# Optimization experiments

Hardware: AMD Instinct MI355X
Metric: run time of the kernel (lower is better)

The kernel has to match this reference:

```python
import jax, jax.numpy as jnp
import numpy as np
from jax import lax


def conv2d(x, w, b=None, pad=0):
    out = lax.conv_general_dilated(x, w, (1, 1), [(pad, pad), (pad, pad)],
                                   dimension_numbers=('NCHW', 'OIHW', 'NCHW'))
    return out if b is None else out + b[None, :, None, None]


def bn_inf(x, gamma, beta, mean, var, eps=1e-5):
    inv = gamma / jnp.sqrt(var + eps)
    return x * inv[None, :, None, None] + (beta - mean * inv)[None, :, None, None]


def silu(x):
    return x * jax.nn.sigmoid(x)


def deform_conv2d(x, offset, weight, groups):
    # torchvision DeformConv2d v1 semantics: kernel 3x3, stride 1, pad 1, dilation 1,
    # one offset group; offset channels interleaved (dy, dx) per kernel tap, row-major taps.
    B, C, H, W = x.shape
    K = 9
    off = offset.reshape(B, K, 2, H, W)
    dy, dx = off[:, :, 0], off[:, :, 1]                      # (B,K,H,W)
    ki = (jnp.arange(K) // 3 - 1).astype(x.dtype)            # kernel row offset (pad=1)
    kj = (jnp.arange(K) % 3 - 1).astype(x.dtype)
    py = jnp.arange(H, dtype=x.dtype)[None, None, :, None] + ki[None, :, None, None] + dy
    px = jnp.arange(W, dtype=x.dtype)[None, None, None, :] + kj[None, :, None, None] + dx
    y0 = jnp.floor(py)
    x0 = jnp.floor(px)
    wy1 = py - y0                                            # bilinear weights
    wx1 = px - x0
    y0i = y0.astype(jnp.int32)
    x0i = x0.astype(jnp.int32)
    xf = x.reshape(B, C, H * W)

    def gather(yi, xi):
        valid = ((yi >= 0) & (yi < H) & (xi >= 0) & (xi < W)).astype(x.dtype)
        idx = (jnp.clip(yi, 0, H - 1) * W + jnp.clip(xi, 0, W - 1)).reshape(B, K * H * W)
        v = jax.vmap(lambda f, i: jnp.take(f, i, axis=-1))(xf, idx).reshape(B, C, K, H, W)
        return v * valid[:, None]

    cols = (gather(y0i, x0i) * ((1 - wy1) * (1 - wx1))[:, None]
            + gather(y0i, x0i + 1) * ((1 - wy1) * wx1)[:, None]
            + gather(y0i + 1, x0i) * (wy1 * (1 - wx1))[:, None]
            + gather(y0i + 1, x0i + 1) * (wy1 * wx1)[:, None])   # (B,C,K,H,W)

    G = groups
    Cg = C // G
    Co = weight.shape[0]
    cols = cols.reshape(B, G, Cg, K, H, W)
    wg = weight.reshape(G, Co // G, Cg, K)
    return jnp.einsum('bgckhw,gock->bgohw', cols, wg).reshape(B, Co, H, W)


def d_clem_forward(x, x_prev, w_off, b_off, w_def, w_cross, w_g1, b_g1,
                   g1_gamma, g1_beta, g1_mean, g1_var, w_g2, b_g2,
                   w_out, b_out, o_gamma, o_beta, o_mean, o_var):
    offset = conv2d(x, w_off, b_off, pad=1)
    x_dir = deform_conv2d(x, offset, w_def, groups=4)
    x_dense = conv2d(jnp.concatenate([x_dir, x_prev], axis=1), w_cross, None, pad=0)
    a = silu(bn_inf(conv2d(x_dense, w_g1, b_g1, pad=1), g1_gamma, g1_beta, g1_mean, g1_var))
    attn = jax.nn.sigmoid(conv2d(a, w_g2, b_g2, pad=0))
    out = silu(bn_inf(conv2d(x_dense * attn, w_out, b_out, pad=0), o_gamma, o_beta, o_mean, o_var))
    return x + out  # use_residual: in_channels == out_channels


def setup_inputs() -> dict:
    key = jax.random.key(0)
    ks = jax.random.split(key, 16)
    B, C, H, W, G = 4, 256, 64, 64, 4

    def wt(k, shape, fan_in):
        return jax.random.normal(k, shape, jnp.float32) / np.float32(np.sqrt(fan_in))

    return {
        'x': jax.random.normal(ks[0], (B, C, H, W), jnp.float32),
        'x_prev': jax.random.normal(ks[1], (B, C, H, W), jnp.float32),
        'w_off': wt(ks[2], (18, C, 3, 3), C * 9),
        'b_off': 0.01 * jax.random.normal(ks[3], (18,), jnp.float32),
        'w_def': wt(ks[4], (C, C // G, 3, 3), (C // G) * 9),
        'w_cross': wt(ks[5], (C, 2 * C, 1, 1), 2 * C),
        'w_g1': wt(ks[6], (C // 4, C, 3, 3), C * 9),
        'b_g1': 0.01 * jax.random.normal(ks[7], (C // 4,), jnp.float32),
        'g1_gamma': 1.0 + 0.1 * jax.random.normal(ks[8], (C // 4,), jnp.float32),
        'g1_beta': 0.1 * jax.random.normal(ks[9], (C // 4,), jnp.float32),
        'g1_mean': 0.1 * jax.random.normal(ks[10], (C // 4,), jnp.float32),
        'g1_var': 0.5 + jax.random.uniform(ks[11], (C // 4,), jnp.float32),
        'w_g2': wt(ks[12], (C, C // 4, 1, 1), C // 4),
        'b_g2': jnp.zeros((C,), jnp.float32),
        'w_out': wt(ks[13], (C, C, 1, 1), C),
        'b_out': jnp.zeros((C,), jnp.float32),
        'o_gamma': 1.0 + 0.1 * jax.random.normal(ks[14], (C,), jnp.float32),
        'o_beta': jnp.zeros((C,), jnp.float32),
        'o_mean': 0.1 * jax.random.normal(ks[15], (C,), jnp.float32),
        'o_var': 0.5 + jax.random.uniform(jax.random.fold_in(key, 99), (C,), jnp.float32),
    }


def reference(x, x_prev, w_off, b_off, w_def, w_cross, w_g1, b_g1,
              g1_gamma, g1_beta, g1_mean, g1_var, w_g2, b_g2,
              w_out, b_out, o_gamma, o_beta, o_mean, o_var):
    return d_clem_forward(x, x_prev, w_off, b_off, w_def, w_cross, w_g1, b_g1,
                          g1_gamma, g1_beta, g1_mean, g1_var, w_g2, b_g2,
                          w_out, b_out, o_gamma, o_beta, o_mean, o_var)
```

## Files before the change

kernel.cpp:

```cpp
#include <hip/hip_runtime.h>
#include <hip/hip_bf16.h>

using bf16 = __hip_bfloat16;
typedef __attribute__((ext_vector_type(8))) short short8;
typedef __attribute__((ext_vector_type(4))) float f32x4;

__device__ __forceinline__ float b2f(bf16 v){ return __bfloat162float(v); }
__device__ __forceinline__ float sigf(float v){ return 1.f/(1.f + __expf(-v)); }
__device__ __forceinline__ float ldv(const float* p, int i){ return p[i]; }
__device__ __forceinline__ float ldv(const bf16* p, int i){ return b2f(p[i]); }
__device__ __forceinline__ void stv(float* p, int i, float v){ p[i] = v; }
__device__ __forceinline__ void stv(bf16* p, int i, float v){ p[i] = __float2bfloat16(v); }
__device__ __forceinline__ float bfe(short8 v, int j){
  unsigned short s = (unsigned short)v[j];
  return b2f(*(bf16*)&s);
}

__device__ __forceinline__ void ld2v(const float* p, float& a, float& b){
  float2 v = *(const float2*)p; a = v.x; b = v.y;
}
__device__ __forceinline__ void ld2v(const bf16* p, float& a, float& b){
  unsigned int u = *(const unsigned int*)p;
  unsigned short s0 = (unsigned short)(u & 0xFFFF), s1 = (unsigned short)(u >> 16);
  a = b2f(*(bf16*)&s0); b = b2f(*(bf16*)&s1);
}
__device__ __forceinline__ void ld8(const bf16* s, unsigned int* pk){
  short8 v = *(const short8*)s;
  #pragma unroll
  for (int e = 0; e < 4; e++)
    pk[e] = (unsigned int)(unsigned short)v[2*e]
          | ((unsigned int)(unsigned short)v[2*e+1] << 16);
}
__device__ __forceinline__ void ld8(const float* s, unsigned int* pk){
  f32x4 a = *(const f32x4*)s, c = *(const f32x4*)(s + 4);
  float vals[8] = {a[0],a[1],a[2],a[3],c[0],c[1],c[2],c[3]};
  #pragma unroll
  for (int e = 0; e < 4; e++){
    bf16 h0 = __float2bfloat16(vals[2*e]), h1 = __float2bfloat16(vals[2*e+1]);
    pk[e] = (unsigned int)*(unsigned short*)&h0
          | ((unsigned int)*(unsigned short*)&h1 << 16);
  }
}

__global__ __launch_bounds__(256) void k_detect(const unsigned short* xs, int* flag){
  __shared__ int cnt;
  if (threadIdx.x == 0) cnt = 0;
  __syncthreads();
  int local = 0;
  for (int i = threadIdx.x; i < 16384; i += 256){
    if (((xs[i] >> 7) & 0xFF) == 0xFF) local++;
  }
  if (local) atomicAdd(&cnt, local);
  __syncthreads();
  if (threadIdx.x == 0) *flag = (cnt > 0) ? 1 : 0;
}

struct ParamSrc { const void* p[18]; };

__global__ __launch_bounds__(256) void k_convert(ParamSrc ps, const int* flagp,
    float* cpar, bf16* wdefb, bf16* woffb, bf16* wg1b, bf16* wcrossb, bf16* woutb,
    float* cwT){
  static constexpr int n[24]   = {41472,18,147456,131072,147456,64,64,64,64,64,
                                  16384,256,65536,256,256,256,256,256,
                                  147456,73728,147456,131072,65536,16384};
  static constexpr int off[18] = {0,41472,41504,188960,320032,467488,467552,467616,
                                  467680,467744,467808,484192,484448,549984,550240,
                                  550496,550752,551008};
  const int s = blockIdx.y;
  const bool f32 = (*flagp != 0);
  if (s == 23){
    for (int i = blockIdx.x * 256 + threadIdx.x; i < 16384; i += gridDim.x * 256){
      const int c = i >> 8, co = i & 255;
      if (f32) cwT[i] = ((const float*)ps.p[10])[co * 64 + c];
      else     cwT[i] = b2f(((const bf16*)ps.p[10])[co * 64 + c]);
    }
    return;
  }
  if (s >= 18){
    static constexpr int srcs[5] = {2, 0, 4, 3, 12};
    const int src_slot = srcs[s - 18];
    bf16* dst = (s == 18) ? wdefb : (s == 19) ? woffb : (s == 20) ? wg1b
              : (s == 21) ? wcrossb : woutb;
    const int nsrc = (s == 19) ? 41472 : n[s];
    const bool remap = (s == 19 || s == 20);
    for (int i = blockIdx.x * 256 + threadIdx.x; i < n[s]; i += gridDim.x * 256){
      int srcIdx = i;
      if (remap){
        const int co = i / 2304, rem = i % 2304;
        const int chunk = rem / 288, r2 = rem % 288;
        const int tap = r2 >> 5, cl = r2 & 31;
        srcIdx = co * 2304 + (chunk * 32 + cl) * 9 + tap;
      }
      if (f32){
        const float* src = (const float*)ps.p[src_slot];
        dst[i] = (srcIdx < nsrc) ? __float2bfloat16(src[srcIdx]) : __float2bfloat16(0.f);
      } else {
        const bf16* src = (const bf16*)ps.p[src_slot];
        dst[i] = (srcIdx < nsrc) ? src[srcIdx] : __float2bfloat16(0.f);
      }
    }
    return;
  }
  float* dst = cpar + off[s];
  if (f32){
    const float* src = (const float*)ps.p[s];
    for (int i = blockIdx.x * 256 + threadIdx.x; i < n[s]; i += gridDim.x * 256)
      dst[i] = src[i];
  } else {
    const bf16* src = (const bf16*)ps.p[s];
    for (int i = blockIdx.x * 256 + threadIdx.x; i < n[s]; i += gridDim.x * 256)
      dst[i] = b2f(src[i]);
  }
}

template<typename T>
__device__ __forceinline__ void xt_body(const T* __restrict__ x, bf16* __restrict__ xt){
  __shared__ float lds[64][65];
  const int bx = blockIdx.x;
  const int b = bx >> 8, y = (bx >> 2) & 63, g = bx & 3;
  const int t = threadIdx.x;
  const int px = t & 63, cq = t >> 6;
  #pragma unroll
  for (int it = 0; it < 16; it++){
    const int ch = cq * 16 + it;
    lds[ch][px] = ldv(x, ((b * 256 + g * 64 + ch) * 64 + y) * 64 + px);
  }
  __syncthreads();
  const int ch = t & 63, pb = t >> 6;
  bf16* ob = xt + ((b * 4 + g) * 4096 + y * 64) * 64 + ch;
  #pragma unroll
  for (int i = 0; i < 16; i++){
    const int p = pb * 16 + i;
    ob[p * 64] = __float2bfloat16(lds[ch][p]);
  }
}

__global__ __launch_bounds__(256) void k_xt(const void* x, const int* flagp, bf16* xt){
  if (*flagp) xt_body((const float*)x, xt);
  else        xt_body((const bf16*)x, xt);
}

template<typename T, int COT>
__device__ __forceinline__ void conv3_raw(const T* __restrict__ xin,
    const bf16* __restrict__ wb, float* __restrict__ outp, int co_lim,
    unsigned short* xt16, int cc_begin){
  const int bx = blockIdx.x;
  const int b = bx >> 6, y = bx & 63;
  const int t = threadIdx.x;
  const int l = t & 63, w = t >> 6;
  const int lm = l & 15, lq = l >> 4;
  const int px = w * 16 + lm;
  f32x4 acc[COT];
  #pragma unroll
  for (int m = 0; m < COT; m++) acc[m] = (f32x4){0.f,0.f,0.f,0.f};

  #pragma unroll
  for (int ch_i = 0; ch_i < 2; ch_i++){
    const int cc = cc_begin + ch_i * 32;
    __syncthreads();
    if (t < 96){
      const int c = t / 3, r = t - c * 3;
      xt16[c * 210 + r * 70 + 3]  = 0;
      xt16[c * 210 + r * 70 + 68] = 0;
    }
    #pragma unroll
    for (int it = 0; it < 3; it++){
      const int u = t + it * 256;
      const int pb = u & 7;
      const int cr = u >> 3;
      const int c = cr / 3, r = cr - c * 3;
      const int yy = y + r - 1;
      const int px0 = pb * 8;
      unsigned int pk[4];
      if ((unsigned)yy < 64u){
        ld8(xin + (b * 256 + cc + c) * 4096 + yy * 64 + px0, pk);
      } else {
        pk[0] = pk[1] = pk[2] = pk[3] = 0;
      }
      unsigned int* dp = (unsigned int*)(xt16 + c * 210 + r * 70 + 4 + px0);
      dp[0] = pk[0]; dp[1] = pk[1]; dp[2] = pk[2]; dp[3] = pk[3];
    }
    __syncthreads();
    const int chunkG = cc >> 5;
    const unsigned short* bt = xt16 + 3 + px;
    #pragma unroll
    for (int tap = 0; tap < 9; tap++){
      const int ti = tap / 3, tj = tap - ti * 3;
      short8 bfr;
      #pragma unroll
      for (int j = 0; j < 8; j++)
        bfr[j] = (short)bt[(lq * 8 + j) * 210 + ti * 70 + tj];
      #pragma unroll
      for (int m = 0; m < COT; m++){
        const bf16* ap = wb + (m * 16 + lm) * 2304 + chunkG * 288 + tap * 32 + lq * 8;
        short8 afr = *(const short8*)ap;
        acc[m] = __builtin_amdgcn_mfma_f32_16x16x32_bf16(afr, bfr, acc[m], 0, 0, 0);
      }
    }
  }
  const int p = y * 64 + px;
  #pragma unroll
  for (int m = 0; m < COT; m++){
    #pragma unroll
    for (int r = 0; r < 4; r++){
      const int co = m * 16 + lq * 4 + r;
      if (co >= co_lim) continue;
      outp[(b * co_lim + co) * 4096 + p] = acc[m][r];
    }
  }
}

__global__ __launch_bounds__(256) void k_coff_m(const void* x, const int* flagp,
    const bf16* woffb, float* offp){
  __shared__ __align__(16) unsigned short xtile[32 * 210];
  float* op = offp + blockIdx.y * 294912;
  const int cc0 = blockIdx.y * 64;
  if (*flagp) conv3_raw<float, 2>((const float*)x, woffb, op, 18, xtile, cc0);
  else        conv3_raw<bf16, 2>((const bf16*)x, woffb, op, 18, xtile, cc0);
}

__global__ __launch_bounds__(256) void k_g1_m(const bf16* xdense,
    const bf16* wg1b, float* abp){
  __shared__ __align__(16) unsigned short xtile[32 * 210];
  float* op = abp + blockIdx.y * 1048576;
  conv3_raw<bf16, 4>(xdense, wg1b, op, 64, xtile, blockIdx.y * 64);
}

__global__ __launch_bounds__(256) void k_omerge(const float* __restrict__ offp,
    const float* __restrict__ cb, float* __restrict__ offc){
  const int i4 = (blockIdx.x * 256 + threadIdx.x) * 4;
  constexpr int PS = 294912;
  f32x4 a = *(const f32x4*)(offp + i4);
  f32x4 b = *(const f32x4*)(offp + PS + i4);
  f32x4 c = *(const f32x4*)(offp + 2 * PS + i4);
  f32x4 d = *(const f32x4*)(offp + 3 * PS + i4);
  const int co = (i4 >> 12) % 18;
  const float bias = cb[co];
  f32x4 r;
  #pragma unroll
  for (int j = 0; j < 4; j++) r[j] = ((a[j] + b[j]) + c[j]) + d[j] + bias;
  *(f32x4*)(offc + i4) = r;
}

#define CROWM 600

__global__ __launch_bounds__(256) void k_deform(const bf16* __restrict__ xt,
    const float* __restrict__ offc, const bf16* __restrict__ wdefb,
    bf16* __restrict__ xdir){
  __shared__ __align__(16) unsigned short cols[32 * CROWM];
  const int g = blockIdx.y;
  const int q0 = blockIdx.x * 32;
  const int b = q0 >> 12, p0 = q0 & 4095;
  const int t = threadIdx.x;
  {
    const int pos = t & 31, u8 = t >> 5;
    const int c0 = u8 * 8;
    const int p = p0 + pos;
    const int y = p >> 6, xx = p & 63;
    const float* ob = offc + b * 18 * 4096 + p;
    const bf16* xg = xt + (b * 4 + g) * 4096 * 64;
    #pragma unroll
    for (int k = 0; k < 9; k++){
      float dy = ob[(2 * k) * 4096];
      float dx = ob[(2 * k + 1) * 4096];
      float py = (float)(y + k / 3 - 1) + dy;
      float px = (float)(xx + k % 3 - 1) + dx;
      float y0f = floorf(py), x0f = floorf(px);
      int y0 = (int)y0f, x0 = (int)x0f;
      float wy1 = py - y0f, wx1 = px - x0f;
      float wy0 = 1.f - wy1, wx0 = 1.f - wx1;
      bool vy0 = (unsigned)y0 < 64u, vy1 = (unsigned)(y0 + 1) < 64u;
      bool vx0 = (unsigned)x0 < 64u, vx1 = (unsigned)(x0 + 1) < 64u;
      float w00 = (vy0 && vx0) ? wy0 * wx0 : 0.f;
      float w01 = (vy0 && vx1) ? wy0 * wx1 : 0.f;
      float w10 = (vy1 && vx0) ? wy1 * wx0 : 0.f;
      float w11 = (vy1 && vx1) ? wy1 * wx1 : 0.f;
      int yc0 = min(max(y0, 0), 63), yc1 = min(max(y0 + 1, 0), 63);
      int xc0 = min(max(x0, 0), 63), xc1 = min(max(x0 + 1, 0), 63);
      int i00 = yc0 * 64 + xc0, i01 = yc0 * 64 + xc1;
      int i10 = yc1 * 64 + xc0, i11 = yc1 * 64 + xc1;
      short8 s00 = *(const short8*)(xg + i00 * 64 + c0);
      short8 s01 = *(const short8*)(xg + i01 * 64 + c0);
      short8 s10 = *(const short8*)(xg + i10 * 64 + c0);
      short8 s11 = *(const short8*)(xg + i11 * 64 + c0);
      #pragma unroll
      for (int j = 0; j < 8; j++){
        float val = w00 * bfe(s00, j) + w01 * bfe(s01, j)
                  + w10 * bfe(s10, j) + w11 * bfe(s11, j);
        bf16 hv = __float2bfloat16(val);
        cols[pos * CROWM + (c0 + j) * 9 + k] = *(unsigned short*)&hv;
      }
    }
  }
  __syncthreads();
  {
    const int w = t >> 6;
    const int l = t & 63;
    const int lrow = l & 15;
    const int lhi = l >> 4;
    f32x4 acc0 = {0.f, 0.f, 0.f, 0.f};
    f32x4 acc1 = {0.f, 0.f, 0.f, 0.f};
    const bf16* wr = wdefb + (g * 64 + w * 16 + lrow) * 576;
    const unsigned short* b0p = cols + lrow * CROWM;
    const unsigned short* b1p = cols + (16 + lrow) * CROWM;
    #pragma unroll 2
    for (int kk = 0; kk < 576; kk += 32){
      int ko = kk + lhi * 8;
      short8 a  = *(const short8*)(wr + ko);
      short8 b0 = *(const short8*)(b0p + ko);
      short8 b1 = *(const short8*)(b1p + ko);
      acc0 = __builtin_amdgcn_mfma_f32_16x16x32_bf16(a, b0, acc0, 0, 0, 0);
      acc1 = __builtin_amdgcn_mfma_f32_16x16x32_bf16(a, b1, acc1, 0, 0, 0);
    }
    const int co_base = g * 64 + w * 16 + lhi * 4;
    #pragma unroll
    for (int r = 0; r < 4; r++){
      bf16* xo = xdir + (b * 256 + co_base + r) * 4096 + p0 + lrow;
      xo[0]  = __float2bfloat16(acc0[r]);
      xo[16] = __float2bfloat16(acc1[r]);
    }
  }
}

template<typename T>
__device__ __forceinline__ void cross_load(const bf16* __restrict__ xdir,
    const T* __restrict__ xprev, int b, int y, int pos2, int cq, int cc,
    unsigned int* pk){
  #pragma unroll
  for (int c8 = 0; c8 < 8; c8++){
    const int ci = cc + cq * 8 + c8;
    if (ci < 256){
      pk[c8] = *(const unsigned int*)(xdir + (b * 256 + ci) * 4096 + y * 64 + 2 * pos2);
    } else {
      float v0, v1;
      ld2v(xprev + (b * 256 + (ci - 256)) * 4096 + y * 64 + 2 * pos2, v0, v1);
      bf16 h0 = __float2bfloat16(v0), h1 = __float2bfloat16(v1);
      pk[c8] = (unsigned int)*(unsigned short*)&h0
             | ((unsigned int)*(unsigned short*)&h1 << 16);
    }
  }
}

template<typename T>
__device__ __forceinline__ void cross_mfma_body(const bf16* __restrict__ xdir,
    const T* __restrict__ xprev, const bf16* __restrict__ wb,
    bf16* __restrict__ xdense, unsigned short* cols){
  const int bx = blockIdx.x;
  const int b = bx >> 6, y = bx & 63;
  const int co0 = blockIdx.y * 64;
  const int t = threadIdx.x;
  const int l = t & 63, w = t >> 6;
  const int lm = l & 15, lq = l >> 4;
  const int pos2 = t & 31, cq = t >> 5;
  unsigned int* cols32 = (unsigned int*)cols;
  f32x4 acc[4];
  #pragma unroll
  for (int m = 0; m < 4; m++) acc[m] = (f32x4){0.f,0.f,0.f,0.f};
  unsigned int pk[8];
  cross_load(xdir, xprev, b, y, pos2, cq, 0, pk);

  for (int c = 0; c < 8; c++){
    __syncthreads();
    #pragma unroll
    for (int c8 = 0; c8 < 8; c8++)
      cols32[(cq * 8 + c8) * 34 + pos2] = pk[c8];
    __syncthreads();
    if (c < 7) cross_load(xdir, xprev, b, y, pos2, cq, (c + 1) * 64, pk);
    const int cc = c * 64;
    #pragma unroll
    for (int kk = 0; kk < 64; kk += 32){
      short8 bfr;
      #pragma unroll
      for (int j = 0; j < 8; j++)
        bfr[j] = (short)cols[(kk + lq * 8 + j) * 68 + w * 16 + lm];
      #pragma unroll
      for (int m = 0; m < 4; m++){
        const bf16* ap = wb + (co0 + m * 16 + lm) * 512 + cc + kk + lq * 8;
        short8 afr = *(const short8*)ap;
        acc[m] = __builtin_amdgcn_mfma_f32_16x16x32_bf16(afr, bfr, acc[m], 0, 0, 0);
      }
    }
  }
  const int p = y * 64 + w * 16 + lm;
  #pragma unroll
  for (int m = 0; m < 4; m++){
    #pragma unroll
    for (int r = 0; r < 4; r++){
      const int co = co0 + m * 16 + lq * 4 + r;
      xdense[(b * 256 + co) * 4096 + p] = __float2bfloat16(acc[m][r]);
    }
  }
}

__global__ __launch_bounds__(256) void k_cross(const bf16* xdir, const void* xprev,
    const int* flagp, const bf16* wcb, bf16* xdense){
  __shared__ __align__(16) unsigned short cols[64 * 68];
  if (*flagp) cross_mfma_body(xdir, (const float*)xprev, wcb, xdense, cols);
  else        cross_mfma_body(xdir, (const bf16*)xprev, wcb, xdense, cols);
}

__global__ __launch_bounds__(256) void k_attn(const float* __restrict__ abp,
    const float* __restrict__ cb1, const float* __restrict__ gam,
    const float* __restrict__ bet, const float* __restrict__ mea,
    const float* __restrict__ var, const float* __restrict__ cwT,
    const float* __restrict__ cb2, const bf16* __restrict__ xdense,
    bf16* __restrict__ xa){
  __shared__ float a_s[64][17];
  const int bx = blockIdx.x;
  const int b = bx >> 8, pc = bx & 255;
  const int p0 = pc * 16;
  const int t = threadIdx.x;
  constexpr int PS = 1048576;
  {
    const int ch = t >> 2;
    const int px0 = (t & 3) * 4;
    const float inv = gam[ch] * rsqrtf(var[ch] + 1e-5f);
    const float sh  = bet[ch] - mea[ch] * inv;
    const float bias = cb1[ch];
    const int ai = (b * 64 + ch) * 4096 + p0 + px0;
    #pragma unroll
    for (int j = 0; j < 4; j++){
      float s = ((abp[ai + j] + abp[PS + ai + j]) + abp[2 * PS + ai + j])
              + abp[3 * PS + ai + j];
      s += bias;
      s = s * inv + sh;
      s = s * sigf(s);
      a_s[ch][px0 + j] = s;
    }
  }
  __syncthreads();
  const int co = t;
  float acc[16];
  #pragma unroll
  for (int i = 0; i < 16; i++) acc[i] = 0.f;
  for (int c = 0; c < 64; c++){
    const float wv = cwT[c * 256 + co];
    #pragma unroll
    for (int i = 0; i < 16; i++) acc[i] += wv * a_s[c][i];
  }
  const float bias2 = cb2[co];
  const int base = (b * 256 + co) * 4096 + p0;
  #pragma unroll
  for (int i = 0; i < 16; i++){
    float attn = sigf(acc[i] + bias2);
    xa[base + i] = __float2bfloat16(b2f(xdense[base + i]) * attn);
  }
}

__device__ __forceinline__ void out_load(const bf16* __restrict__ xa,
    int b, int y, int pos2, int cq, int cc, unsigned int* pk){
  #pragma unroll
  for (int c8 = 0; c8 < 8; c8++){
    const int ci = cc + cq * 8 + c8;
    pk[c8] = *(const unsigned int*)(xa + (b * 256 + ci) * 4096 + y * 64 + 2 * pos2);
  }
}

template<typename T>
__device__ __forceinline__ void out_mfma_body(const bf16* __restrict__ xa,
    const bf16* __restrict__ wb, const float* __restrict__ cbv,
    const float* __restrict__ gam, const float* __restrict__ bet,
    const float* __restrict__ mea, const float* __restrict__ var,
    const T* __restrict__ xres, T* __restrict__ outp, unsigned short* cols){
  const int bx = blockIdx.x;
  const int b = bx >> 6, y = bx & 63;
  const int co0 = blockIdx.y * 64;
  const int t = threadIdx.x;
  const int l = t & 63, w = t >> 6;
  const int lm = l & 15, lq = l >> 4;
  const int pos2 = t & 31, cq = t >> 5;
  unsigned int* cols32 = (unsigned int*)cols;
  f32x4 acc[4];
  #pragma unroll
  for (int m = 0; m < 4; m++) acc[m] = (f32x4){0.f,0.f,0.f,0.f};
  unsigned int pk[8];
  out_load(xa, b, y, pos2, cq, 0, pk);

  for (int c = 0; c < 4; c++){
    __syncthreads();
    #pragma unroll
    for (int c8 = 0; c8 < 8; c8++)
      cols32[(cq * 8 + c8) * 34 + pos2] = pk[c8];
    __syncthreads();
    if (c < 3) out_load(xa, b, y, pos2, cq, (c + 1) * 64, pk);
    const int cc = c * 64;
    #pragma unroll
    for (int kk = 0; kk < 64; kk += 32){
      short8 bfr;
      #pragma unroll
      for (int j = 0; j < 8; j++)
        bfr[j] = (short)cols[(kk + lq * 8 + j) * 68 + w * 16 + lm];
      #pragma unroll
      for (int m = 0; m < 4; m++){
        const bf16* ap = wb + (co0 + m * 16 + lm) * 256 + cc + kk + lq * 8;
        short8 afr = *(const short8*)ap;
        acc[m] = __builtin_amdgcn_mfma_f32_16x16x32_bf16(afr, bfr, acc[m], 0, 0, 0);
      }
    }
  }
  const int p = y * 64 + w * 16 + lm;
  #pragma unroll
  for (int m = 0; m < 4; m++){
    #pragma unroll
    for (int r = 0; r < 4; r++){
      const int co = co0 + m * 16 + lq * 4 + r;
      float inv = gam[co] * rsqrtf(var[co] + 1e-5f);
      float v = acc[m][r] + cbv[co];
      v = v * inv + (bet[co] - mea[co] * inv);
      v = v * sigf(v);
      const int idx = (b * 256 + co) * 4096 + p;
      stv(outp, idx, v + ldv(xres, idx));
    }
  }
}

__global__ __launch_bounds__(256) void k_out(const bf16* xa, const bf16* wob,
    const float* cb, const float* gam, const float* bet, const float* mea,
    const float* var, const void* xres, void* out, const int* flagp){
  __shared__ __align__(16) unsigned short cols[64 * 68];
  if (*flagp) out_mfma_body(xa, wob, cb, gam, bet, mea, var,
                            (const float*)xres, (float*)out, cols);
  else        out_mfma_body(xa, wob, cb, gam, bet, mea, var,
                            (const bf16*)xres, (bf16*)out, cols);
}

extern "C" void kernel_launch(void* const* d_in, const int* in_sizes, int n_in,
                              void* d_out, int out_size, void* d_ws, size_t ws_size,
                              hipStream_t stream) {
  const void* x      = d_in[0];
  const void* x_prev = d_in[1];

  float* ws   = (float*)d_ws;
  int*   flag = (int*)ws;
  float* cpar = ws + 16;
  float* cb_off   = cpar + 41472;
  float* cb_g1    = cpar + 467488;
  float* cg1_gam  = cpar + 467552;
  float* cg1_bet  = cpar + 467616;
  float* cg1_mea  = cpar + 467680;
  float* cg1_var  = cpar + 467744;
  float* cb_g2    = cpar + 484192;
  float* cb_out   = cpar + 549984;
  float* co_gam   = cpar + 550240;
  float* co_bet   = cpar + 550496;
  float* co_mea   = cpar + 550752;
  float* co_var   = cpar + 551008;

  float* cwT     = ws + 16 + 551264;
  bf16*  wdefb   = (bf16*)(ws + 567664);
  bf16*  woffb   = (bf16*)(ws + 641392);
  bf16*  wg1b    = (bf16*)(ws + 678256);
  bf16*  wcrossb = (bf16*)(ws + 751984);
  bf16*  woutb   = (bf16*)(ws + 817520);
  float* base    = ws + 850288;
  float* offp    = base;
  float* offc    = offp + 1179648;
  float* abp     = offc + 294912;
  bf16*  xdirb   = (bf16*)(abp + 4194304);
  bf16*  xdenseb = (bf16*)(abp + 6291456);
  bf16*  xtb     = (bf16*)(abp + 8388608);
  bf16*  xab     = xdirb;

  ParamSrc ps;
  for (int i = 0; i < 18; i++) ps.p[i] = d_in[2 + i];

  k_detect<<<dim3(1), 256, 0, stream>>>((const unsigned short*)x, flag);
  k_convert<<<dim3(96, 24), 256, 0, stream>>>(ps, flag, cpar, wdefb, woffb,
                                              wg1b, wcrossb, woutb, cwT);
  k_xt<<<dim3(1024), 256, 0, stream>>>(x, flag, xtb);
  k_coff_m<<<dim3(256, 4), 256, 0, stream>>>(x, flag, woffb, offp);
  k_omerge<<<dim3(288), 256, 0, stream>>>(offp, cb_off, offc);
  k_deform<<<dim3(512, 4), 256, 0, stream>>>(xtb, offc, wdefb, xdirb);
  k_cross<<<dim3(256, 4), 256, 0, stream>>>(xdirb, x_prev, flag, wcrossb, xdenseb);
  k_g1_m<<<dim3(256, 4), 256, 0, stream>>>(xdenseb, wg1b, abp);
  k_attn<<<dim3(1024), 256, 0, stream>>>(abp, cb_g1, cg1_gam, cg1_bet, cg1_mea,
                                         cg1_var, cwT, cb_g2, xdenseb, xab);
  k_out<<<dim3(256, 4), 256, 0, stream>>>(xab, woutb, cb_out, co_gam, co_bet,
                                          co_mea, co_var, x, d_out, flag);
}
```

Baseline: 328.5 us.

## Reorder deform weights tap-major, vectorize cols stores, prefetch conv3 input chunk

The deformable-conv weight repack now uses a tap-major, channel-inner order. This lets the bilinear sampling loop pack eight bf16 results into a single 16-byte LDS store instead of eight scattered 2-byte stores. The 3x3 conv also loads the second 32-channel input chunk into registers while MFMAs run on the first, overlapping the global load with compute. The changes add register pressure and depend on the cols layout matching the new weight order in the GEMM.

```diff
diff --git a/kernel.cpp b/kernel.cpp
--- a/kernel.cpp
+++ b/kernel.cpp
@@ -4,6 +4,7 @@
 using bf16 = __hip_bfloat16;
 typedef __attribute__((ext_vector_type(8))) short short8;
 typedef __attribute__((ext_vector_type(4))) float f32x4;
+typedef __attribute__((ext_vector_type(4))) unsigned int u32x4;
 
 __device__ __forceinline__ float b2f(bf16 v){ return __bfloat162float(v); }
 __device__ __forceinline__ float sigf(float v){ return 1.f/(1.f + __expf(-v)); }
@@ -82,14 +83,17 @@
     bf16* dst = (s == 18) ? wdefb : (s == 19) ? woffb : (s == 20) ? wg1b
               : (s == 21) ? wcrossb : woutb;
     const int nsrc = (s == 19) ? 41472 : n[s];
-    const bool remap = (s == 19 || s == 20);
     for (int i = blockIdx.x * 256 + threadIdx.x; i < n[s]; i += gridDim.x * 256){
       int srcIdx = i;
-      if (remap){
+      if (s == 19 || s == 20){
         const int co = i / 2304, rem = i % 2304;
         const int chunk = rem / 288, r2 = rem % 288;
         const int tap = r2 >> 5, cl = r2 & 31;
         srcIdx = co * 2304 + (chunk * 32 + cl) * 9 + tap;
+      } else if (s == 18){
+        const int co = i / 576, rem = i % 576;
+        const int tap = rem >> 6, c = rem & 63;
+        srcIdx = co * 576 + c * 9 + tap;
       }
       if (f32){
         const float* src = (const float*)ps.p[src_slot];
@@ -138,6 +142,24 @@
 __global__ __launch_bounds__(256) void k_xt(const void* x, const int* flagp, bf16* xt){
   if (*flagp) xt_body((const float*)x, xt);
   else        xt_body((const bf16*)x, xt);
+}
+
+template<typename T, int COT>
+__device__ __forceinline__ void conv3_load(const T* __restrict__ xin,
+    int b, int y, int cc, int t, unsigned int pk[3][4]){
+  #pragma unroll
+  for (int it = 0; it < 3; it++){
+    const int u = t + it * 256;
+    const int pb = u & 7;
+    const int cr = u >> 3;
+    const int c = cr / 3, r = cr - c * 3;
+    const int yy = y + r - 1;
+    if ((unsigned)yy < 64u){
+      ld8(xin + (b * 256 + cc + c) * 4096 + yy * 64 + pb * 8, pk[it]);
+    } else {
+      pk[it][0] = pk[it][1] = pk[it][2] = pk[it][3] = 0;
+    }
+  }
 }
 
 template<typename T, int COT>
@@ -153,10 +175,11 @@
   f32x4 acc[COT];
   #pragma unroll
   for (int m = 0; m < COT; m++) acc[m] = (f32x4){0.f,0.f,0.f,0.f};
+  unsigned int pk[3][4];
+  conv3_load<T, COT>(xin, b, y, cc_begin, t, pk);
 
   #pragma unroll
   for (int ch_i = 0; ch_i < 2; ch_i++){
-    const int cc = cc_begin + ch_i * 32;
     __syncthreads();
     if (t < 96){
       const int c = t / 3, r = t - c * 3;
@@ -169,19 +192,12 @@
       const int pb = u & 7;
       const int cr = u >> 3;
       const int c = cr / 3, r = cr - c * 3;
-      const int yy = y + r - 1;
-      const int px0 = pb * 8;
-      unsigned int pk[4];
-      if ((unsigned)yy < 64u){
-        ld8(xin + (b * 256 + cc + c) * 4096 + yy * 64 + px0, pk);
-      } else {
-        pk[0] = pk[1] = pk[2] = pk[3] = 0;
-      }
-      unsigned int* dp = (unsigned int*)(xt16 + c * 210 + r * 70 + 4 + px0);
-      dp[0] = pk[0]; dp[1] = pk[1]; dp[2] = pk[2]; dp[3] = pk[3];
+      unsigned int* dp = (unsigned int*)(xt16 + c * 210 + r * 70 + 4 + pb * 8);
+      dp[0] = pk[it][0]; dp[1] = pk[it][1]; dp[2] = pk[it][2]; dp[3] = pk[it][3];
     }
     __syncthreads();
-    const int chunkG = cc >> 5;
+    if (ch_i == 0) conv3_load<T, COT>(xin, b, y, cc_begin + 32, t, pk);
+    const int chunkG = (cc_begin + ch_i * 32) >> 5;
     const unsigned short* bt = xt16 + 3 + px;
     #pragma unroll
     for (int tap = 0; tap < 9; tap++){
@@ -283,13 +299,18 @@
       short8 s01 = *(const short8*)(xg + i01 * 64 + c0);
       short8 s10 = *(const short8*)(xg + i10 * 64 + c0);
       short8 s11 = *(const short8*)(xg + i11 * 64 + c0);
+      u32x4 pkv;
       #pragma unroll
-      for (int j = 0; j < 8; j++){
-        float val = w00 * bfe(s00, j) + w01 * bfe(s01, j)
-                  + w10 * bfe(s10, j) + w11 * bfe(s11, j);
-        bf16 hv = __float2bfloat16(val);
-        cols[pos * CROWM + (c0 + j) * 9 + k] = *(unsigned short*)&hv;
+      for (int e = 0; e < 4; e++){
+        float v0 = w00 * bfe(s00, 2*e)   + w01 * bfe(s01, 2*e)
+                 + w10 * bfe(s10, 2*e)   + w11 * bfe(s11, 2*e);
+        float v1 = w00 * bfe(s00, 2*e+1) + w01 * bfe(s01, 2*e+1)
+                 + w10 * bfe(s10, 2*e+1) + w11 * bfe(s11, 2*e+1);
+        bf16 h0 = __float2bfloat16(v0), h1 = __float2bfloat16(v1);
+        pkv[e] = (unsigned int)*(unsigned short*)&h0
+               | ((unsigned int)*(unsigned short*)&h1 << 16);
       }
+      *(u32x4*)(cols + pos * CROWM + k * 64 + c0) = pkv;
     }
   }
   __syncthreads();
```

Result: slower. 336.4 us (+2.4%).
